# Kernel tuning notes

Hardware: AMD Instinct MI355X
Metric: run time of the kernel (lower is better)

## Reference

```python
import jax, jax.numpy as jnp
import numpy as np

N_NODES = 8192
N_EDGES = 262144
N_ADJ = 2
BATCH = 16
D_IN = 32
D_OUT = 64
D_EMB = 64


def setup_inputs() -> dict:
    key = jax.random.key(0)
    ks = jax.random.split(key, 6)
    edge_row = jax.random.randint(ks[0], (N_ADJ, N_EDGES), 0, N_NODES, dtype=jnp.int32)
    edge_col = jax.random.randint(ks[1], (N_ADJ, N_EDGES), 0, N_NODES, dtype=jnp.int32)
    edge_w = jax.random.uniform(ks[2], (N_ADJ, N_EDGES), dtype=jnp.float32)
    X = jax.random.normal(ks[3], (BATCH, D_IN, N_NODES), dtype=jnp.float32)
    Z = jax.random.normal(ks[4], (N_NODES, D_EMB), dtype=jnp.float32)
    stdv = 1.0 / np.sqrt(D_OUT)
    W = jax.random.uniform(ks[5], (D_IN, D_OUT), dtype=jnp.float32, minval=-stdv, maxval=stdv)
    return {"edge_row": edge_row, "edge_col": edge_col, "edge_w": edge_w,
            "X": X, "Z": Z, "W": W}


def reference(edge_row, edge_col, edge_w, X, Z, W):
    batch, d, n = X.shape
    X0 = X.reshape(-1, n)  # [b*d, n]

    def spmm(row, col, w, V):
        # sparse A @ V with A in COO form; V: [n, m] -> [n, m]
        return jax.ops.segment_sum(w[:, None] * V[col], row, num_segments=n)

    terms = [X0]
    for k in range(edge_row.shape[0]):  # small fixed loop over supports
        X1 = spmm(edge_row[k], edge_col[k], edge_w[k], X0.T).T  # [b*d, n]
        X2 = 2.0 * spmm(edge_row[k], edge_col[k], edge_w[k], X1.T).T - X0
        terms += [X1, X2]

    # adaptive adjacency: column-normalized softmax of relu(Z Z^T)
    Az = jax.nn.softmax(jax.nn.relu(Z @ Z.T), axis=0)  # [n, n]
    Xz = (Az @ X0.T).T  # [b*d, n]
    terms.append(Xz)

    Xcat = jnp.stack(terms, axis=2)  # [b*d, n, 2*nA+2]
    Xs = Xcat.sum(2).reshape(batch, d, n).transpose(0, 2, 1)  # [batch, n, d]
    return Xs @ W  # [batch, n, out_features]
```

## Files before the change

kernel.cpp:

```cpp
#include <hip/hip_runtime.h>

#define NN 8192
#define NE 262144
#define BD 512
#define DE 64

typedef __attribute__((ext_vector_type(8))) short short8;
typedef __attribute__((ext_vector_type(4))) short short4v;
typedef __attribute__((ext_vector_type(16))) float float16;

#define MFMA(a, b, c) __builtin_amdgcn_mfma_f32_32x32x16_bf16(a, b, c, 0, 0, 0)

static __device__ __forceinline__ unsigned short f2b(float x) {
  unsigned u = __float_as_uint(x);
  return (unsigned short)((u + 0x7fffu + ((u >> 16) & 1u)) >> 16);
}
static __device__ __forceinline__ float b2f(unsigned short h) {
  return __uint_as_float(((unsigned)h) << 16);
}

__global__ void k_transpose(const float* __restrict__ X, float* __restrict__ Y0,
                            float* __restrict__ Ysum) {
  __shared__ float t[32][33];
  int n0 = blockIdx.x * 32, f0 = blockIdx.y * 32;
  int tx = threadIdx.x, ty = threadIdx.y;
#pragma unroll
  for (int yy = 0; yy < 4; yy++)
    t[ty + 8 * yy][tx] = X[(size_t)(f0 + ty + 8 * yy) * NN + n0 + tx];
  __syncthreads();
#pragma unroll
  for (int yy = 0; yy < 4; yy++) {
    float v = t[tx][ty + 8 * yy];
    size_t o = (size_t)(n0 + ty + 8 * yy) * BD + f0 + tx;
    Y0[o] = v;
    Ysum[o] = -v;
  }
}

__global__ void k_cast(const float* __restrict__ X, unsigned short* __restrict__ Y0bT) {
  size_t t = (size_t)(blockIdx.x * 256 + threadIdx.x) * 8;
  float4 a = *(const float4*)(X + t);
  float4 b = *(const float4*)(X + t + 4);
  short8 v;
  v[0] = (short)f2b(a.x); v[1] = (short)f2b(a.y);
  v[2] = (short)f2b(a.z); v[3] = (short)f2b(a.w);
  v[4] = (short)f2b(b.x); v[5] = (short)f2b(b.y);
  v[6] = (short)f2b(b.z); v[7] = (short)f2b(b.w);
  *(short8*)(Y0bT + t) = v;
}

__global__ void k_zsplit(const float* __restrict__ Z, unsigned short* __restrict__ Zh,
                         unsigned short* __restrict__ Zl) {
  size_t t = (size_t)(blockIdx.x * 256 + threadIdx.x) * 4;
  float4 a = *(const float4*)(Z + t);
  float f[4] = {a.x, a.y, a.z, a.w};
  short4v hv, lv;
#pragma unroll
  for (int i = 0; i < 4; i++) {
    unsigned short hh = f2b(f[i]);
    hv[i] = (short)hh;
    lv[i] = (short)f2b(f[i] - b2f(hh));
  }
  *(short4v*)(Zh + t) = hv;
  *(short4v*)(Zl + t) = lv;
}

__global__ __launch_bounds__(256) void k_colsum(const unsigned short* __restrict__ Zh,
                                                const unsigned short* __restrict__ Zl,
                                                float* __restrict__ ssum) {
  int jt = blockIdx.x;
  int chunk = blockIdx.y;
  int tid = threadIdx.x;
  int w = tid >> 6, lane = tid & 63, li = lane & 31, h = lane >> 5;
  int jb = jt * 64 + (w & 1) * 32 + li;
  short8 bjh[4], bjl[4];
#pragma unroll
  for (int ks = 0; ks < 4; ks++) {
    bjh[ks] = *(const short8*)(Zh + (size_t)jb * DE + ks * 16 + 8 * h);
    bjl[ks] = *(const short8*)(Zl + (size_t)jb * DE + ks * 16 + 8 * h);
  }
  float csum = 0.f;
  for (int it = 0; it < 32; it++) {
    int ib = chunk * 2048 + (w >> 1) * 32 + it * 64 + li;
    short8 aih[4], ail[4];
#pragma unroll
    for (int ks = 0; ks < 4; ks++) {
      aih[ks] = *(const short8*)(Zh + (size_t)ib * DE + ks * 16 + 8 * h);
      ail[ks] = *(const short8*)(Zl + (size_t)ib * DE + ks * 16 + 8 * h);
    }
    float16 s;
#pragma unroll
    for (int r = 0; r < 16; r++) s[r] = 0.f;
#pragma unroll
    for (int ks = 0; ks < 4; ks++) {
      s = MFMA(aih[ks], bjh[ks], s);
      s = MFMA(aih[ks], bjl[ks], s);
      s = MFMA(ail[ks], bjh[ks], s);
    }
#pragma unroll
    for (int r = 0; r < 16; r++)
      csum += __expf(fminf(fmaxf(s[r], 0.f), 80.f));
  }
  csum += __shfl_xor(csum, 32);
  if (lane < 32) atomicAdd(ssum + jb, csum);
}

__global__ void k_inv(const float* __restrict__ ssum, float* __restrict__ invs) {
  int i = blockIdx.x * 256 + threadIdx.x;
  invs[i] = 1.0f / ssum[i];
}

__global__ void k_hist(const int* __restrict__ erow, int* __restrict__ cnt) {
  int t = blockIdx.x * 256 + threadIdx.x;
  int k = t >> 18;
  atomicAdd(cnt + k * NN + erow[t], 1);
}

#define RPS 8208
__global__ __launch_bounds__(256) void k_scan(const int* __restrict__ cnt,
                                              int* __restrict__ rowptr,
                                              int* __restrict__ fill) {
  int k = blockIdx.x;
  const int* c = cnt + k * NN;
  int* rp = rowptr + k * RPS;
  int* fl = fill + k * NN;
  __shared__ int part[256];
  int t = threadIdx.x;
  int local[32];
  int s = 0;
#pragma unroll
  for (int i = 0; i < 32; i++) { local[i] = c[t * 32 + i]; s += local[i]; }
  part[t] = s;
  __syncthreads();
  for (int off = 1; off < 256; off <<= 1) {
    int v = (t >= off) ? part[t - off] : 0;
    __syncthreads();
    part[t] += v;
    __syncthreads();
  }
  int run = (t == 0) ? 0 : part[t - 1];
#pragma unroll
  for (int i = 0; i < 32; i++) {
    rp[t * 32 + i] = run;
    fl[t * 32 + i] = run;
    run += local[i];
  }
  if (t == 255) rp[NN] = run;
}

__global__ void k_scatter(const int* __restrict__ erow, const int* __restrict__ ecol,
                          const float* __restrict__ ew, int* __restrict__ fill,
                          int* __restrict__ ecol_s, float* __restrict__ ew_s) {
  int t = blockIdx.x * 256 + threadIdx.x;
  int k = t >> 18;
  int r = erow[t];
  int pos = atomicAdd(fill + k * NN + r, 1);
  ecol_s[(size_t)k * NE + pos] = ecol[t];
  ew_s[(size_t)k * NE + pos] = ew[t];
}

__global__ __launch_bounds__(256) void k_csr(const int* __restrict__ rowptr,
                                             const int* __restrict__ cols,
                                             const float* __restrict__ w,
                                             const float* __restrict__ src,
                                             float* __restrict__ dst,
                                             const float* __restrict__ extra,
                                             float scale) {
  int wid = threadIdx.x >> 6;
  int lane = threadIdx.x & 63;
  int row = blockIdx.x * 4 + wid;
  int start = rowptr[row], end = rowptr[row + 1];
  float a0x = 0.f, a0y = 0.f, a0z = 0.f, a0w = 0.f;
  float a1x = 0.f, a1y = 0.f, a1z = 0.f, a1w = 0.f;
  for (int e = start; e < end; e++) {
    int c = __builtin_amdgcn_readfirstlane(cols[e]);
    float wv = w[e];
    const float4* s = (const float4*)(src + (size_t)c * BD);
    float4 v0 = s[lane], v1 = s[lane + 64];
    a0x += wv * v0.x; a0y += wv * v0.y; a0z += wv * v0.z; a0w += wv * v0.w;
    a1x += wv * v1.x; a1y += wv * v1.y; a1z += wv * v1.z; a1w += wv * v1.w;
  }
  float4* d = (float4*)(dst + (size_t)row * BD);
  if (extra) {
    const float4* ex = (const float4*)(extra + (size_t)row * BD);
    float4 e0 = ex[lane], e1 = ex[lane + 64];
    float4 d0 = d[lane], d1 = d[lane + 64];
    d0.x += scale * a0x + e0.x; d0.y += scale * a0y + e0.y;
    d0.z += scale * a0z + e0.z; d0.w += scale * a0w + e0.w;
    d1.x += scale * a1x + e1.x; d1.y += scale * a1y + e1.y;
    d1.z += scale * a1z + e1.z; d1.w += scale * a1w + e1.w;
    d[lane] = d0; d[lane + 64] = d1;
  } else {
    float4 d0 = {a0x, a0y, a0z, a0w};
    float4 d1 = {a1x, a1y, a1z, a1w};
    d[lane] = d0; d[lane + 64] = d1;
  }
}

__global__ __launch_bounds__(256, 2) void k2(const unsigned short* __restrict__ Zh,
                                             const unsigned short* __restrict__ Zl,
                                             const unsigned short* __restrict__ Y0bT,
                                             const float* __restrict__ invs,
                                             float* __restrict__ Ysum) {
  __shared__ float red[4][32][33];
  int bid = blockIdx.x;
  int fhalf = bid & 1;
  int itile = bid >> 1;
  int i0 = itile * 32;
  int f0 = fhalf * 256;
  int tid = threadIdx.x;
  int w = tid >> 6, lane = tid & 63, li = lane & 31, h = lane >> 5;

  short8 bih[4], bil[4];
#pragma unroll
  for (int ks = 0; ks < 4; ks++) {
    bih[ks] = *(const short8*)(Zh + (size_t)(i0 + li) * DE + ks * 16 + 8 * h);
    bil[ks] = *(const short8*)(Zl + (size_t)(i0 + li) * DE + ks * 16 + 8 * h);
  }
  float16 acc[8];
#pragma unroll
  for (int ft = 0; ft < 8; ft++)
#pragma unroll
    for (int r = 0; r < 16; r++) acc[ft][r] = 0.f;

#pragma unroll 1
  for (int t = 0; t < 64; t++) {
    int jb = t * 128 + w * 32;
    short8 ajh[4], ajl[4];
#pragma unroll
    for (int ks = 0; ks < 4; ks++) {
      ajh[ks] = *(const short8*)(Zh + (size_t)(jb + li) * DE + ks * 16 + 8 * h);
      ajl[ks] = *(const short8*)(Zl + (size_t)(jb + li) * DE + ks * 16 + 8 * h);
    }
    float16 s;
#pragma unroll
    for (int r = 0; r < 16; r++) s[r] = 0.f;
#pragma unroll
    for (int ks = 0; ks < 4; ks++) {
      s = MFMA(ajh[ks], bih[ks], s);
      s = MFMA(ajh[ks], bil[ks], s);
      s = MFMA(ajl[ks], bih[ks], s);
    }
    unsigned wds[8];
#pragma unroll
    for (int q = 0; q < 8; q++) {
      int r0 = q * 2;
      int jl0 = 2 * (q & 1) + 8 * (q >> 1) + 4 * h;
      float iv0 = invs[jb + jl0];
      float iv1 = invs[jb + jl0 + 1];
      float p0 = __expf(fminf(fmaxf(s[r0], 0.f), 80.f)) * iv0;
      float p1 = __expf(fminf(fmaxf(s[r0 + 1], 0.f), 80.f)) * iv1;
      asm("v_cvt_pk_bf16_f32 %0, %1, %2" : "=v"(wds[q]) : "v"(p0), "v"(p1));
    }
#pragma unroll
    for (int ks2 = 0; ks2 < 2; ks2++) {
      unsigned A0 = wds[ks2 * 4 + 0], A1 = wds[ks2 * 4 + 1];
      unsigned A2 = wds[ks2 * 4 + 2], A3 = wds[ks2 * 4 + 3];
      asm("v_permlane32_swap_b32 %0, %1" : "+v"(A0), "+v"(A2));
      asm("v_permlane32_swap_b32 %0, %1" : "+v"(A1), "+v"(A3));
      union { unsigned u[4]; short8 s8; } fu;
      fu.u[0] = A0; fu.u[1] = A1; fu.u[2] = A2; fu.u[3] = A3;
#pragma unroll
      for (int ft = 0; ft < 8; ft++) {
        const unsigned short* bp =
            Y0bT + (size_t)(f0 + ft * 32 + li) * NN + jb + ks2 * 16 + 8 * h;
        short8 B = *(const short8*)bp;
        acc[ft] = MFMA(fu.s8, B, acc[ft]);
      }
    }
  }
#pragma unroll 1
  for (int ft = 0; ft < 8; ft++) {
    __syncthreads();
#pragma unroll
    for (int r = 0; r < 16; r++) {
      int ir = (r & 3) + 8 * (r >> 2) + 4 * h;
      red[w][ir][li] = acc[ft][r];
    }
    __syncthreads();
#pragma unroll
    for (int q = 0; q < 4; q++) {
      int e = q * 256 + tid;
      int row = e >> 5, col = e & 31;
      float sv = red[0][row][col] + red[1][row][col] +
                 red[2][row][col] + red[3][row][col];
      Ysum[(size_t)(i0 + row) * BD + f0 + ft * 32 + col] += sv;
    }
  }
}

__global__ void k3(const float* __restrict__ Ysum, const float* __restrict__ W,
                   float* __restrict__ out) {
  __shared__ float yt[32][68];
  __shared__ float wt[32][68];
  int n0 = blockIdx.x * 64;
  int b = blockIdx.y;
  int tid = threadIdx.x;
#pragma unroll
  for (int q = 0; q < 2; q++) {
    int flat = (q * 256 + tid) * 4;
    int r = flat >> 5, c = flat & 31;
    float4 a = *(const float4*)(Ysum + (size_t)(n0 + r) * BD + b * 32 + c);
    yt[c + 0][r] = a.x; yt[c + 1][r] = a.y; yt[c + 2][r] = a.z; yt[c + 3][r] = a.w;
    int rd = flat >> 6, co = flat & 63;
    *(float4*)&wt[rd][co] = *(const float4*)(W + rd * 64 + co);
  }
  __syncthreads();
  int tx = tid & 15, ty = tid >> 4;
  float acc[4][4];
#pragma unroll
  for (int a = 0; a < 4; a++)
#pragma unroll
    for (int bq = 0; bq < 4; bq++) acc[a][bq] = 0.f;
#pragma unroll
  for (int d = 0; d < 32; d++) {
    float4 a = *(const float4*)&yt[d][ty * 4];
    float4 w4 = *(const float4*)&wt[d][tx * 4];
    float av[4] = {a.x, a.y, a.z, a.w}, wv[4] = {w4.x, w4.y, w4.z, w4.w};
#pragma unroll
    for (int nn = 0; nn < 4; nn++)
#pragma unroll
      for (int oo = 0; oo < 4; oo++) acc[nn][oo] += av[nn] * wv[oo];
  }
#pragma unroll
  for (int nn = 0; nn < 4; nn++) {
    float4 v = {acc[nn][0], acc[nn][1], acc[nn][2], acc[nn][3]};
    *(float4*)(out + (size_t)b * NN * 64 + (size_t)(n0 + ty * 4 + nn) * 64 + tx * 4) = v;
  }
}

extern "C" void kernel_launch(void* const* d_in, const int* in_sizes, int n_in,
                              void* d_out, int out_size, void* d_ws, size_t ws_size,
                              hipStream_t stream) {
  const int* erow = (const int*)d_in[0];
  const int* ecol = (const int*)d_in[1];
  const float* ew = (const float*)d_in[2];
  const float* X = (const float*)d_in[3];
  const float* Z = (const float*)d_in[4];
  const float* W = (const float*)d_in[5];
  float* out = (float*)d_out;

  char* p = (char*)d_ws;
  float* Y0 = (float*)p;                     p += (size_t)NN * BD * 4;
  float* Ysum = (float*)p;                   p += (size_t)NN * BD * 4;
  float* Y1 = (float*)p;                     p += (size_t)NN * BD * 4;
  unsigned short* Y0bT = (unsigned short*)p; p += (size_t)BD * NN * 2;
  unsigned short* Zh = (unsigned short*)p;   p += (size_t)NN * DE * 2;
  unsigned short* Zl = (unsigned short*)p;   p += (size_t)NN * DE * 2;
  float* ssum = (float*)p;                   p += NN * 4;
  float* invs = (float*)p;                   p += NN * 4;
  int* cnt = (int*)p;                        p += 2 * NN * 4;
  int* rowptr = (int*)p;                     p += 2 * RPS * 4;
  int* fill = (int*)p;                       p += 2 * NN * 4;
  int* ecol_s = (int*)p;                     p += (size_t)2 * NE * 4;
  float* ew_s = (float*)p;                   p += (size_t)2 * NE * 4;

  k_transpose<<<dim3(NN / 32, BD / 32), dim3(32, 8), 0, stream>>>(X, Y0, Ysum);
  k_zsplit<<<(NN * DE / 4) / 256, 256, 0, stream>>>(Z, Zh, Zl);
  hipMemsetAsync(ssum, 0, NN * sizeof(float), stream);
  hipMemsetAsync(cnt, 0, 2 * NN * sizeof(int), stream);
  k_hist<<<2 * NE / 256, 256, 0, stream>>>(erow, cnt);
  k_scan<<<2, 256, 0, stream>>>(cnt, rowptr, fill);
  k_scatter<<<2 * NE / 256, 256, 0, stream>>>(erow, ecol, ew, fill, ecol_s, ew_s);
  k_colsum<<<dim3(128, 4), 256, 0, stream>>>(Zh, Zl, ssum);
  k_inv<<<NN / 256, 256, 0, stream>>>(ssum, invs);
  for (int k = 0; k < 2; k++) {
    const int* rp = rowptr + k * RPS;
    const int* cs = ecol_s + (size_t)k * NE;
    const float* ws = ew_s + (size_t)k * NE;
    k_csr<<<NN / 4, 256, 0, stream>>>(rp, cs, ws, Y0, Y1, nullptr, 1.0f);
    k_csr<<<NN / 4, 256, 0, stream>>>(rp, cs, ws, Y1, Ysum, Y1, 2.0f);
  }
  k_cast<<<(NN * BD / 8) / 256, 256, 0, stream>>>(X, Y0bT);
  k2<<<512, 256, 0, stream>>>(Zh, Zl, Y0bT, invs, Ysum);
  k3<<<dim3(NN / 64, 16), 256, 0, stream>>>(Ysum, W, out);
}
```

Measured before the change: 913.2 us.

## Retile attention GEMM to 64 rows x 128 features with blocked X layout

The k2 kernel now processes 64 output nodes and 128 features per block instead of 32 nodes and 256 features, so each loaded X tile feeds two MFMAs. The Z-tile loads are also shared across two i-fragments. The cast kernel writes X into a blocked [n/32][feature][32] bf16 layout, which makes each B-fragment load contiguous. Blocks also start the j-loop at staggered phases to spread L2 traffic. The cost is that the exp/softmax and Z·Z MFMA work per i row stays the same while registers per thread go up, which may put pressure on the occupancy of 2 blocks.

```diff
diff --git a/kernel.cpp b/kernel.cpp
--- a/kernel.cpp
+++ b/kernel.cpp
@@ -37,16 +37,20 @@
   }
 }
 
-__global__ void k_cast(const float* __restrict__ X, unsigned short* __restrict__ Y0bT) {
-  size_t t = (size_t)(blockIdx.x * 256 + threadIdx.x) * 8;
-  float4 a = *(const float4*)(X + t);
-  float4 b = *(const float4*)(X + t + 4);
+__global__ void k_castB(const float* __restrict__ X, unsigned short* __restrict__ Y0bB) {
+  int t = blockIdx.x * 256 + threadIdx.x;
+  int f = t >> 10;
+  int n0 = (t & 1023) * 8;
+  const float* src = X + (size_t)f * NN + n0;
+  float4 a = *(const float4*)(src);
+  float4 b = *(const float4*)(src + 4);
   short8 v;
   v[0] = (short)f2b(a.x); v[1] = (short)f2b(a.y);
   v[2] = (short)f2b(a.z); v[3] = (short)f2b(a.w);
   v[4] = (short)f2b(b.x); v[5] = (short)f2b(b.y);
   v[6] = (short)f2b(b.z); v[7] = (short)f2b(b.w);
-  *(short8*)(Y0bT + t) = v;
+  size_t o = ((size_t)(n0 >> 5) * BD + f) * 32 + (n0 & 31);
+  *(short8*)(Y0bB + o) = v;
 }
 
 __global__ void k_zsplit(const float* __restrict__ Z, unsigned short* __restrict__ Zh,
@@ -199,83 +203,100 @@
 
 __global__ __launch_bounds__(256, 2) void k2(const unsigned short* __restrict__ Zh,
                                              const unsigned short* __restrict__ Zl,
-                                             const unsigned short* __restrict__ Y0bT,
+                                             const unsigned short* __restrict__ Y0bB,
                                              const float* __restrict__ invs,
                                              float* __restrict__ Ysum) {
   __shared__ float red[4][32][33];
   int bid = blockIdx.x;
-  int fhalf = bid & 1;
-  int itile = bid >> 1;
-  int i0 = itile * 32;
-  int f0 = fhalf * 256;
+  int fq = bid & 3;
+  int itile = bid >> 2;
+  int i0 = itile * 64;
+  int f0 = fq * 128;
+  int phase = itile & 63;
   int tid = threadIdx.x;
   int w = tid >> 6, lane = tid & 63, li = lane & 31, h = lane >> 5;
 
-  short8 bih[4], bil[4];
-#pragma unroll
-  for (int ks = 0; ks < 4; ks++) {
-    bih[ks] = *(const short8*)(Zh + (size_t)(i0 + li) * DE + ks * 16 + 8 * h);
-    bil[ks] = *(const short8*)(Zl + (size_t)(i0 + li) * DE + ks * 16 + 8 * h);
-  }
-  float16 acc[8];
-#pragma unroll
-  for (int ft = 0; ft < 8; ft++)
-#pragma unroll
-    for (int r = 0; r < 16; r++) acc[ft][r] = 0.f;
+  short8 bih[2][4], bil[2][4];
+#pragma unroll
+  for (int ifr = 0; ifr < 2; ifr++)
+#pragma unroll
+    for (int ks = 0; ks < 4; ks++) {
+      bih[ifr][ks] = *(const short8*)(Zh + (size_t)(i0 + ifr * 32 + li) * DE + ks * 16 + 8 * h);
+      bil[ifr][ks] = *(const short8*)(Zl + (size_t)(i0 + ifr * 32 + li) * DE + ks * 16 + 8 * h);
+    }
+  float16 acc[4][2];
+#pragma unroll
+  for (int ft = 0; ft < 4; ft++)
+#pragma unroll
+    for (int ifr = 0; ifr < 2; ifr++)
+#pragma unroll
+      for (int r = 0; r < 16; r++) acc[ft][ifr][r] = 0.f;
 
 #pragma unroll 1
-  for (int t = 0; t < 64; t++) {
+  for (int tt = 0; tt < 64; tt++) {
+    int t = (tt + phase) & 63;
     int jb = t * 128 + w * 32;
-    short8 ajh[4], ajl[4];
+    int jt = t * 4 + w;
+    float16 s0, s1;
+#pragma unroll
+    for (int r = 0; r < 16; r++) { s0[r] = 0.f; s1[r] = 0.f; }
 #pragma unroll
     for (int ks = 0; ks < 4; ks++) {
-      ajh[ks] = *(const short8*)(Zh + (size_t)(jb + li) * DE + ks * 16 + 8 * h);
-      ajl[ks] = *(const short8*)(Zl + (size_t)(jb + li) * DE + ks * 16 + 8 * h);
-    }
-    float16 s;
-#pragma unroll
-    for (int r = 0; r < 16; r++) s[r] = 0.f;
-#pragma unroll
-    for (int ks = 0; ks < 4; ks++) {
-      s = MFMA(ajh[ks], bih[ks], s);
-      s = MFMA(ajh[ks], bil[ks], s);
-      s = MFMA(ajl[ks], bih[ks], s);
-    }
-    unsigned wds[8];
+      short8 ajh = *(const short8*)(Zh + (size_t)(jb + li) * DE + ks * 16 + 8 * h);
+      short8 ajl = *(const short8*)(Zl + (size_t)(jb + li) * DE + ks * 16 + 8 * h);
+      s0 = MFMA(ajh, bih[0][ks], s0);
+      s0 = MFMA(ajh, bil[0][ks], s0);
+      s0 = MFMA(ajl, bih[0][ks], s0);
+      s1 = MFMA(ajh, bih[1][ks], s1);
+      s1 = MFMA(ajh, bil[1][ks], s1);
+      s1 = MFMA(ajl, bih[1][ks], s1);
+    }
+    unsigned wds0[8], wds1[8];
 #pragma unroll
     for (int q = 0; q < 8; q++) {
       int r0 = q * 2;
       int jl0 = 2 * (q & 1) + 8 * (q >> 1) + 4 * h;
       float iv0 = invs[jb + jl0];
       float iv1 = invs[jb + jl0 + 1];
-      float p0 = __expf(fminf(fmaxf(s[r0], 0.f), 80.f)) * iv0;
-      float p1 = __expf(fminf(fmaxf(s[r0 + 1], 0.f), 80.f)) * iv1;
-      asm("v_cvt_pk_bf16_f32 %0, %1, %2" : "=v"(wds[q]) : "v"(p0), "v"(p1));
+      float p0 = __expf(fminf(fmaxf(s0[r0], 0.f), 80.f)) * iv0;
+      float p1 = __expf(fminf(fmaxf(s0[r0 + 1], 0.f), 80.f)) * iv1;
+      asm("v_cvt_pk_bf16_f32 %0, %1, %2" : "=v"(wds0[q]) : "v"(p0), "v"(p1));
+      float p2 = __expf(fminf(fmaxf(s1[r0], 0.f), 80.f)) * iv0;
+      float p3 = __expf(fminf(fmaxf(s1[r0 + 1], 0.f), 80.f)) * iv1;
+      asm("v_cvt_pk_bf16_f32 %0, %1, %2" : "=v"(wds1[q]) : "v"(p2), "v"(p3));
     }
 #pragma unroll
     for (int ks2 = 0; ks2 < 2; ks2++) {
-      unsigned A0 = wds[ks2 * 4 + 0], A1 = wds[ks2 * 4 + 1];
-      unsigned A2 = wds[ks2 * 4 + 2], A3 = wds[ks2 * 4 + 3];
+      unsigned A0 = wds0[ks2 * 4 + 0], A1 = wds0[ks2 * 4 + 1];
+      unsigned A2 = wds0[ks2 * 4 + 2], A3 = wds0[ks2 * 4 + 3];
       asm("v_permlane32_swap_b32 %0, %1" : "+v"(A0), "+v"(A2));
       asm("v_permlane32_swap_b32 %0, %1" : "+v"(A1), "+v"(A3));
-      union { unsigned u[4]; short8 s8; } fu;
-      fu.u[0] = A0; fu.u[1] = A1; fu.u[2] = A2; fu.u[3] = A3;
-#pragma unroll
-      for (int ft = 0; ft < 8; ft++) {
+      union { unsigned u[4]; short8 s8; } fu0;
+      fu0.u[0] = A0; fu0.u[1] = A1; fu0.u[2] = A2; fu0.u[3] = A3;
+      unsigned B0 = wds1[ks2 * 4 + 0], B1 = wds1[ks2 * 4 + 1];
+      unsigned B2 = wds1[ks2 * 4 + 2], B3 = wds1[ks2 * 4 + 3];
+      asm("v_permlane32_swap_b32 %0, %1" : "+v"(B0), "+v"(B2));
+      asm("v_permlane32_swap_b32 %0, %1" : "+v"(B1), "+v"(B3));
+      union { unsigned u[4]; short8 s8; } fu1;
+      fu1.u[0] = B0; fu1.u[1] = B1; fu1.u[2] = B2; fu1.u[3] = B3;
+#pragma unroll
+      for (int ft = 0; ft < 4; ft++) {
         const unsigned short* bp =
-            Y0bT + (size_t)(f0 + ft * 32 + li) * NN + jb + ks2 * 16 + 8 * h;
+            Y0bB + ((size_t)jt * BD + f0 + ft * 32 + li) * 32 + ks2 * 16 + 8 * h;
         short8 B = *(const short8*)bp;
-        acc[ft] = MFMA(fu.s8, B, acc[ft]);
+        acc[ft][0] = MFMA(fu0.s8, B, acc[ft][0]);
+        acc[ft][1] = MFMA(fu1.s8, B, acc[ft][1]);
       }
     }
   }
 #pragma unroll 1
-  for (int ft = 0; ft < 8; ft++) {
+  for (int fi = 0; fi < 8; fi++) {
+    int ft = fi >> 1, ifr = fi & 1;
     __syncthreads();
 #pragma unroll
     for (int r = 0; r < 16; r++) {
       int ir = (r & 3) + 8 * (r >> 2) + 4 * h;
-      red[w][ir][li] = acc[ft][r];
+      red[w][ir][li] = acc[ft][ifr][r];
     }
     __syncthreads();
 #pragma unroll
@@ -284,7 +305,7 @@
       int row = e >> 5, col = e & 31;
       float sv = red[0][row][col] + red[1][row][col] +
                  red[2][row][col] + red[3][row][col];
-      Ysum[(size_t)(i0 + row) * BD + f0 + ft * 32 + col] += sv;
+      Ysum[(size_t)(i0 + ifr * 32 + row) * BD + f0 + ft * 32 + col] += sv;
     }
   }
 }
@@ -344,7 +365,7 @@
   float* Y0 = (float*)p;                     p += (size_t)NN * BD * 4;
   float* Ysum = (float*)p;                   p += (size_t)NN * BD * 4;
   float* Y1 = (float*)p;                     p += (size_t)NN * BD * 4;
-  unsigned short* Y0bT = (unsigned short*)p; p += (size_t)BD * NN * 2;
+  unsigned short* Y0bB = (unsigned short*)p; p += (size_t)BD * NN * 2;
   unsigned short* Zh = (unsigned short*)p;   p += (size_t)NN * DE * 2;
   unsigned short* Zl = (unsigned short*)p;   p += (size_t)NN * DE * 2;
   float* ssum = (float*)p;                   p += NN * 4;
@@ -371,7 +392,7 @@
     k_csr<<<NN / 4, 256, 0, stream>>>(rp, cs, ws, Y0, Y1, nullptr, 1.0f);
     k_csr<<<NN / 4, 256, 0, stream>>>(rp, cs, ws, Y1, Ysum, Y1, 2.0f);
   }
-  k_cast<<<(NN * BD / 8) / 256, 256, 0, stream>>>(X, Y0bT);
-  k2<<<512, 256, 0, stream>>>(Zh, Zl, Y0bT, invs, Ysum);
+  k_castB<<<(NN * BD / 8) / 256, 256, 0, stream>>>(X, Y0bB);
+  k2<<<512, 256, 0, stream>>>(Zh, Zl, Y0bB, invs, Ysum);
   k3<<<dim3(NN / 64, 16), 256, 0, stream>>>(Ysum, W, out);
 }
```

Result: faster. 804.2 us (-11.9%).

## Block X bf16 into node tiles, split dense k2 over four feature quarters

Applied to the files above, without the earlier changes.

The bf16 copy of X is now stored in 32-node blocks ([n/32][feature][32]) so each k2 B-fragment load reads a contiguous chunk instead of striding by NN. k2 is split over four feature quarters (1024 blocks, 4 accumulators instead of 8), and each tile starts its j-loop at a staggered phase so blocks do not all hit the same rows at once. The loop is also unrolled by 2. The gain is better memory locality, more parallelism and fewer registers. The cost is that the Z·Z^T scores and exponentials are recomputed twice as often.

```diff
diff --git a/kernel.cpp b/kernel.cpp
--- a/kernel.cpp
+++ b/kernel.cpp
@@ -37,16 +37,20 @@
   }
 }
 
-__global__ void k_cast(const float* __restrict__ X, unsigned short* __restrict__ Y0bT) {
-  size_t t = (size_t)(blockIdx.x * 256 + threadIdx.x) * 8;
-  float4 a = *(const float4*)(X + t);
-  float4 b = *(const float4*)(X + t + 4);
+__global__ void k_castB(const float* __restrict__ X, unsigned short* __restrict__ Y0bB) {
+  int t = blockIdx.x * 256 + threadIdx.x;
+  int f = t >> 10;
+  int n0 = (t & 1023) * 8;
+  const float* src = X + (size_t)f * NN + n0;
+  float4 a = *(const float4*)(src);
+  float4 b = *(const float4*)(src + 4);
   short8 v;
   v[0] = (short)f2b(a.x); v[1] = (short)f2b(a.y);
   v[2] = (short)f2b(a.z); v[3] = (short)f2b(a.w);
   v[4] = (short)f2b(b.x); v[5] = (short)f2b(b.y);
   v[6] = (short)f2b(b.z); v[7] = (short)f2b(b.w);
-  *(short8*)(Y0bT + t) = v;
+  size_t o = ((size_t)(n0 >> 5) * BD + f) * 32 + (n0 & 31);
+  *(short8*)(Y0bB + o) = v;
 }
 
 __global__ void k_zsplit(const float* __restrict__ Z, unsigned short* __restrict__ Zh,
@@ -199,15 +203,16 @@
 
 __global__ __launch_bounds__(256, 2) void k2(const unsigned short* __restrict__ Zh,
                                              const unsigned short* __restrict__ Zl,
-                                             const unsigned short* __restrict__ Y0bT,
+                                             const unsigned short* __restrict__ Y0bB,
                                              const float* __restrict__ invs,
                                              float* __restrict__ Ysum) {
   __shared__ float red[4][32][33];
   int bid = blockIdx.x;
-  int fhalf = bid & 1;
-  int itile = bid >> 1;
+  int fq = bid & 3;
+  int itile = bid >> 2;
   int i0 = itile * 32;
-  int f0 = fhalf * 256;
+  int f0 = fq * 128;
+  int phase = itile & 63;
   int tid = threadIdx.x;
   int w = tid >> 6, lane = tid & 63, li = lane & 31, h = lane >> 5;
 
@@ -217,15 +222,17 @@
     bih[ks] = *(const short8*)(Zh + (size_t)(i0 + li) * DE + ks * 16 + 8 * h);
     bil[ks] = *(const short8*)(Zl + (size_t)(i0 + li) * DE + ks * 16 + 8 * h);
   }
-  float16 acc[8];
-#pragma unroll
-  for (int ft = 0; ft < 8; ft++)
+  float16 acc[4];
+#pragma unroll
+  for (int ft = 0; ft < 4; ft++)
 #pragma unroll
     for (int r = 0; r < 16; r++) acc[ft][r] = 0.f;
 
-#pragma unroll 1
-  for (int t = 0; t < 64; t++) {
+#pragma unroll 2
+  for (int tt = 0; tt < 64; tt++) {
+    int t = (tt + phase) & 63;
     int jb = t * 128 + w * 32;
+    int jt = t * 4 + w;
     short8 ajh[4], ajl[4];
 #pragma unroll
     for (int ks = 0; ks < 4; ks++) {
@@ -261,16 +268,16 @@
       union { unsigned u[4]; short8 s8; } fu;
       fu.u[0] = A0; fu.u[1] = A1; fu.u[2] = A2; fu.u[3] = A3;
 #pragma unroll
-      for (int ft = 0; ft < 8; ft++) {
+      for (int ft = 0; ft < 4; ft++) {
         const unsigned short* bp =
-            Y0bT + (size_t)(f0 + ft * 32 + li) * NN + jb + ks2 * 16 + 8 * h;
+            Y0bB + ((size_t)jt * BD + f0 + ft * 32 + li) * 32 + ks2 * 16 + 8 * h;
         short8 B = *(const short8*)bp;
         acc[ft] = MFMA(fu.s8, B, acc[ft]);
       }
     }
   }
 #pragma unroll 1
-  for (int ft = 0; ft < 8; ft++) {
+  for (int ft = 0; ft < 4; ft++) {
     __syncthreads();
 #pragma unroll
     for (int r = 0; r < 16; r++) {
@@ -344,7 +351,7 @@
   float* Y0 = (float*)p;                     p += (size_t)NN * BD * 4;
   float* Ysum = (float*)p;                   p += (size_t)NN * BD * 4;
   float* Y1 = (float*)p;                     p += (size_t)NN * BD * 4;
-  unsigned short* Y0bT = (unsigned short*)p; p += (size_t)BD * NN * 2;
+  unsigned short* Y0bB = (unsigned short*)p; p += (size_t)BD * NN * 2;
   unsigned short* Zh = (unsigned short*)p;   p += (size_t)NN * DE * 2;
   unsigned short* Zl = (unsigned short*)p;   p += (size_t)NN * DE * 2;
   float* ssum = (float*)p;                   p += NN * 4;
@@ -371,7 +378,7 @@
     k_csr<<<NN / 4, 256, 0, stream>>>(rp, cs, ws, Y0, Y1, nullptr, 1.0f);
     k_csr<<<NN / 4, 256, 0, stream>>>(rp, cs, ws, Y1, Ysum, Y1, 2.0f);
   }
-  k_cast<<<(NN * BD / 8) / 256, 256, 0, stream>>>(X, Y0bT);
-  k2<<<512, 256, 0, stream>>>(Zh, Zl, Y0bT, invs, Ysum);
+  k_castB<<<(NN * BD / 8) / 256, 256, 0, stream>>>(X, Y0bB);
+  k2<<<1024, 256, 0, stream>>>(Zh, Zl, Y0bB, invs, Ysum);
   k3<<<dim3(NN / 64, 16), 256, 0, stream>>>(Ysum, W, out);
 }
```

Result: slower. 1.014 ms (+11.0%).
